# Performance work log

Measured on AMD Instinct MI355X. Metric: run time of the kernel, lower is better.

## Reference

```python
import jax, jax.numpy as jnp
import numpy as np

T_MAX, BATCH, NUM_CLASSES = 128, 64, 32
BEAM = 16
BLANK_DEC = NUM_CLASSES - 1   # TF ctc_beam_search_decoder uses num_classes-1 as blank
BLANK_PAD = 0                 # layer's blank_index: pad value for the dense output
NEG = -1e30                   # finite -inf substitute (avoids nan in logsumexp)


def setup_inputs():
    key = jax.random.key(0)
    k1, k2 = jax.random.split(key)
    data = jax.random.normal(k1, (T_MAX, BATCH, NUM_CLASSES), dtype=jnp.float32)
    data_length = jax.random.randint(k2, (BATCH,), T_MAX // 2, T_MAX + 1).astype(jnp.int32)
    return {"data": data, "data_length": data_length}


def _decode_one(logp_seq, length):
    """CTC prefix beam search (Graves) for one sample.
    logp_seq: [T, C] log-softmax scores. length: scalar int valid frames.
    Returns (dense prediction [T] padded with BLANK_PAD, log prob of best path).
    """
    Tt, Cc = logp_seq.shape
    L = Tt  # max decoded length
    bw = BEAM
    ar_b = jnp.arange(bw)
    ar_c = jnp.arange(Cc)
    ar_l = jnp.arange(L)

    prefixes0 = jnp.zeros((bw, L), jnp.int32)
    lens0 = jnp.zeros((bw,), jnp.int32)
    lp_b0 = jnp.full((bw,), NEG, jnp.float32).at[0].set(0.0)  # empty prefix, ends in blank
    lp_nb0 = jnp.full((bw,), NEG, jnp.float32)

    def step(state, inp):
        prefixes, lens, lp_b, lp_nb = state
        logp, t = inp
        lp_tot = jnp.logaddexp(lp_b, lp_nb)                      # [bw]
        valid = lp_tot > NEG / 2                                 # live beams (prefixes distinct)
        last = jnp.where(lens > 0, prefixes[ar_b, jnp.maximum(lens - 1, 0)], -1)

        # -- 'stay' candidates: prefix unchanged (emit blank, or repeat last char) --
        stay_lp_b = lp_tot + logp[BLANK_DEC]
        stay_lp_nb = jnp.where(lens > 0, lp_nb + logp[jnp.maximum(last, 0)], NEG)

        # -- 'extend' candidates ext[i, c]: prefix_i ++ [c], c != blank --
        # repeating last char only continues from the blank-ending mass
        ext = jnp.where(ar_c[None, :] == last[:, None], lp_b[:, None], lp_tot[:, None]) + logp[None, :]
        ext = ext.at[:, BLANK_DEC].set(NEG)

        # -- merge ext(i, c) into stay(j) when prefixes[j] == prefixes[i] ++ [c] --
        eq = prefixes[:, None, :] == prefixes[None, :, :]        # [i, j, L]
        maskp = ar_l[None, None, :] < lens[:, None, None]        # positions p < lens[i]
        pm = jnp.all(eq | ~maskp, axis=-1)                       # [i, j] prefix match up to lens[i]
        char_ji = prefixes[:, jnp.minimum(lens, L - 1)].T        # [i, j] = prefixes[j, lens[i]]
        match = (pm & (lens[None, :] == lens[:, None] + 1) & valid[None, :])[:, :, None] \
                & (char_ji[:, :, None] == ar_c[None, None, :])   # [i, j, C]
        merged = jax.nn.logsumexp(jnp.where(match, ext[:, None, :], NEG), axis=(0, 2))  # [j]
        stay_lp_nb = jnp.logaddexp(stay_lp_nb, merged)
        consumed = jnp.any(match, axis=1)                        # [i, C]
        ext = jnp.where(consumed, NEG, ext)

        # -- keep top beam_width candidates (all remaining prefixes are distinct) --
        stay_score = jnp.logaddexp(stay_lp_b, stay_lp_nb)        # [bw]
        scores = jnp.concatenate([stay_score, ext.reshape(-1)])  # [bw + bw*C]
        _, idx = jax.lax.top_k(scores, bw)
        is_ext = idx >= bw
        i_stay = jnp.minimum(idx, bw - 1)
        e = jnp.maximum(idx - bw, 0)
        i_ext, c_ext = e // Cc, e % Cc
        src = jnp.where(is_ext, i_ext, i_stay)
        base_pref = prefixes[src]                                # [bw, L]
        base_len = lens[src]
        new_pref = jnp.where(is_ext[:, None] & (ar_l[None, :] == base_len[:, None]),
                             c_ext[:, None].astype(jnp.int32), base_pref)
        new_len = base_len + is_ext.astype(jnp.int32)
        new_lp_b = jnp.where(is_ext, NEG, stay_lp_b[i_stay])
        new_lp_nb = jnp.where(is_ext, ext[i_ext, c_ext], stay_lp_nb[i_stay])

        # frames past this sample's length leave the state untouched
        active = t < length
        prefixes = jnp.where(active, new_pref, prefixes)
        lens = jnp.where(active, new_len, lens)
        lp_b = jnp.where(active, new_lp_b, lp_b)
        lp_nb = jnp.where(active, new_lp_nb, lp_nb)
        return (prefixes, lens, lp_b, lp_nb), None

    (prefixes, lens, lp_b, lp_nb), _ = jax.lax.scan(
        step, (prefixes0, lens0, lp_b0, lp_nb0), (logp_seq, jnp.arange(Tt)))

    # beam 0 is the most likely path (top_k keeps beams sorted by score);
    # dense output padded with blank_index, mirroring sparse.to_dense + pad
    pred = jnp.where(ar_l < lens[0], prefixes[0], BLANK_PAD)
    prob = jnp.logaddexp(lp_b[0], lp_nb[0])
    return pred, prob


def reference(data, data_length):
    # TF's ctc_beam_search_decoder applies softmax to the logits internally
    logp = jax.nn.log_softmax(data, axis=-1)                     # [T, B, C]
    preds, probs = jax.vmap(_decode_one, in_axes=(1, 0))(logp, data_length)
    # top_paths=1 -> _select_most_likely_path returns the single decoded path
    return preds                                                 # [B, T] int32
```

## Files before the change

kernel.cpp:

```cpp
#include <hip/hip_runtime.h>
#include <math.h>

#define T_MAXX 128
#define BATCHN 64
#define NC     32
#define NCP    33
#define BW     16
#define BLANKC 31
#define NEGF   (-1e30f)

typedef unsigned long long u64;
typedef unsigned int u32;

static const u64 PA_C = 0x100000001B3ULL;
static const u64 PB_C = 6364136223846793005ULL;

#define FENCE() asm volatile("" ::: "memory")

__device__ __forceinline__ float xexp(float x)  { return expf(x); }
__device__ __forceinline__ float xlog(float x)  { return logf(x); }
__device__ __forceinline__ float xlog1p(float x){ return log1pf(x); }

__device__ __forceinline__ float logaddexpf_(float a, float b) {
    float m = fmaxf(a, b);
    float d = fabsf(a - b);
    return m + xlog1p(xexp(-d));
}

template<int C>
__device__ __forceinline__ float fdpp_keep(float v) {
    return __int_as_float(__builtin_amdgcn_update_dpp(
        __float_as_int(v), __float_as_int(v), C, 0xF, 0xF, false));
}
template<int C>
__device__ __forceinline__ float fdpp_zero(float v) {
    return __int_as_float(__builtin_amdgcn_update_dpp(
        0, __float_as_int(v), C, 0xF, 0xF, true));
}
template<int C>
__device__ __forceinline__ u32 udpp_keep(u32 v) {
    return (u32)__builtin_amdgcn_update_dpp((int)v, (int)v, C, 0xF, 0xF, false);
}

__device__ __forceinline__ double dkey_pack(u32 u, u32 inv10) {
    u64 p = 0x3FF0000000000000ULL | ((u64)u << 10) | (u64)inv10;
    return __longlong_as_double((long long)p);
}
template<int C>
__device__ __forceinline__ double ddpp_keep(double v) {
    u64 b = (u64)__double_as_longlong(v);
    u32 lo = udpp_keep<C>((u32)b);
    u32 hi = udpp_keep<C>((u32)(b >> 32));
    return __longlong_as_double((long long)(((u64)hi << 32) | lo));
}
template<int P>
__device__ __forceinline__ double dswz(double v) {
    u64 b = (u64)__double_as_longlong(v);
    u32 lo = (u32)__builtin_amdgcn_ds_swizzle((int)(u32)b, P);
    u32 hi = (u32)__builtin_amdgcn_ds_swizzle((int)(u32)(b >> 32), P);
    return __longlong_as_double((long long)(((u64)hi << 32) | lo));
}
__device__ __forceinline__ double dbperm(double v, int srcl) {
    u64 b = (u64)__double_as_longlong(v);
    u32 lo = (u32)__builtin_amdgcn_ds_bpermute(srcl << 2, (int)(u32)b);
    u32 hi = (u32)__builtin_amdgcn_ds_bpermute(srcl << 2, (int)(u32)(b >> 32));
    return __longlong_as_double((long long)(((u64)hi << 32) | lo));
}
__device__ __forceinline__ double grp16_dmax(double m) {
    m = fmax(m, ddpp_keep<0xB1>(m));
    m = fmax(m, ddpp_keep<0x4E>(m));
    m = fmax(m, ddpp_keep<0x141>(m));
    m = fmax(m, ddpp_keep<0x140>(m));
    return m;
}
__device__ __forceinline__ void dce(double &m, double o, bool keepmax) {
    double mx = fmax(m, o), mn = fmin(m, o);
    m = keepmax ? mx : mn;
}

extern "C" __global__ void __launch_bounds__(64)
CTCPredictionsCpu_kernel(const float* __restrict__ data,
                         const int* __restrict__ dlen,
                         int* __restrict__ out)
{
    const int b      = blockIdx.x;
    const int tid    = threadIdx.x;
    const int length = dlen[b];
    const int lane_c = tid & 31;
    const int lane_h = tid >> 5;
    const int lane_g = tid & 15;
    const int grp    = tid >> 4;

    __shared__ float logpS[T_MAXX][NC];
    __shared__ float ext[BW][NCP];
    __shared__ int   lensS[BW], lastS[BW];
    __shared__ float lpBS[BW], lpTotS[BW];
    __shared__ u64   hAS[BW], hBS[BW];
    __shared__ u64   hAXS[BW], hBXS[BW];
    __shared__ int   trace[T_MAXX][BW];
    __shared__ int   outbuf[T_MAXX];

    #pragma unroll 4
    for (int f0 = 0; f0 < T_MAXX; f0 += 2) {
        int f = f0 + lane_h;
        float x = data[((size_t)f * BATCHN + b) * NC + lane_c];
        float mm = x;
        mm = fmaxf(mm, fdpp_keep<0xB1>(mm));
        mm = fmaxf(mm, fdpp_keep<0x4E>(mm));
        mm = fmaxf(mm, fdpp_keep<0x141>(mm));
        mm = fmaxf(mm, fdpp_keep<0x140>(mm));
        { float o = __int_as_float(
              __builtin_amdgcn_ds_swizzle(__float_as_int(mm), 0x401F));
          mm = fmaxf(mm, o); }
        float e = xexp(x - mm);
        float ss = e;
        ss += fdpp_zero<0xB1>(ss);
        ss += fdpp_zero<0x4E>(ss);
        ss += fdpp_zero<0x141>(ss);
        ss += fdpp_zero<0x140>(ss);
        { float o = __int_as_float(
              __builtin_amdgcn_ds_swizzle(__float_as_int(ss), 0x401F));
          ss += o; }
        float ls2 = xlog(ss);
        logpS[f][lane_c] = (x - mm) - ls2;
    }
    FENCE();

    int   myLen  = 0;
    int   myLast = -1;
    float myLpB  = (tid == 0) ? 0.0f : NEGF;
    float myLpNB = NEGF;
    u64   myHA   = 1, myHB = 1;

    for (int t = 0; t < length; ++t) {
        float mylogp  = logpS[t][lane_c];
        float lpBlank = logpS[t][BLANKC];

        float myTot = 0.0f, stayB = 0.0f, stayNB = 0.0f;
        if (tid < BW) {
            myTot = logaddexpf_(myLpB, myLpNB);
            float lp_last = logpS[t][(myLast >= 0) ? myLast : 0];
            stayB  = myTot + lpBlank;
            stayNB = (myLen > 0) ? (myLpNB + lp_last) : NEGF;
            lensS[tid]  = myLen;
            lastS[tid]  = myLast;
            lpBS[tid]   = myLpB;
            lpTotS[tid] = myTot;
            hAS[tid]    = myHA;
            hBS[tid]    = myHB;
            hAXS[tid]   = myHA * PA_C;
            hBXS[tid]   = myHB * PB_C;
        }
        FENCE();

        #pragma unroll
        for (int s8 = 0; s8 < 8; ++s8) {
            int i = 2 * s8 + lane_h;
            float base = (lane_c == lastS[i]) ? lpBS[i] : lpTotS[i];
            float v = base + mylogp;
            if (lane_c == BLANKC) v = NEGF;
            ext[i][lane_c] = v;
        }
        FENCE();

        float staySc = NEGF;
        if (tid < BW) {
            bool valid = myTot > -5e29f;
            if (valid && myLen > 0) {
                const int cj = myLast;
                const u64 wantA = myHA - (u64)(cj + 1);
                const u64 wantB = myHB - (u64)(cj + 1);
                u32 mmask = 0;
                #pragma unroll
                for (int i = 0; i < BW; ++i) {
                    bool hit = (hAXS[i] == wantA) && (hBXS[i] == wantB);
                    mmask |= hit ? (1u << i) : 0u;
                }
                if (mmask) {
                    int i0 = __ffs(mmask) - 1;
                    float merged = ext[i0][cj];
                    ext[i0][cj] = NEGF;
                    stayNB = logaddexpf_(stayNB, merged);
                }
            }
            staySc = logaddexpf_(stayB, stayNB);
        }
        FENCE();

        double K[9];
        #pragma unroll
        for (int j = 0; j < 8; ++j) {
            int r = 4 * grp + (j >> 1);
            int c = lane_g + ((j & 1) << 4);
            u32 uu = __float_as_uint(ext[r][c]);
            uu = (uu & 0x80000000u) ? ~uu : (uu | 0x80000000u);
            K[j] = dkey_pack(uu, 1023u - (u32)(BW + r * NC + c));
        }
        if (grp == 0) {
            u32 u = __float_as_uint(staySc);
            u = (u & 0x80000000u) ? ~u : (u | 0x80000000u);
            K[8] = dkey_pack(u, 1023u - (u32)lane_g);
        } else {
            K[8] = 0.0;
        }

        #define CE(a,bb) { double hi_ = fmax(K[a], K[bb]); \
                           double lo_ = fmin(K[a], K[bb]); \
                           K[a] = hi_; K[bb] = lo_; }
        CE(0,1) CE(2,3) CE(4,5) CE(6,7)
        CE(0,2) CE(1,3) CE(4,6) CE(5,7)
        CE(1,2) CE(5,6)
        CE(0,4) CE(1,5) CE(2,6) CE(3,7)
        CE(2,4) CE(3,5)
        CE(1,2) CE(3,4) CE(5,6)
        CE(7,8) CE(6,7) CE(5,6) CE(4,5) CE(3,4) CE(2,3) CE(1,2) CE(0,1)
        #undef CE

        double W = 0.0;
        #pragma unroll
        for (int k = 0; k < BW; ++k) {
            double best = grp16_dmax(K[0]);
            W = (lane_g == k) ? best : W;
            bool win = (K[0] == best);
            #pragma unroll
            for (int r = 0; r < 8; ++r) K[r] = win ? K[r + 1] : K[r];
            K[8] = win ? 0.0 : K[8];
        }

        { double o = dswz<0x7C1F>(W);    dce(W, o, (tid & 16) == 0); }
        { double o = dswz<0x201F>(W);    dce(W, o, (tid & 8)  == 0); }
        { double o = dswz<0x101F>(W);    dce(W, o, (tid & 4)  == 0); }
        { double o = ddpp_keep<0x4E>(W); dce(W, o, (tid & 2)  == 0); }
        { double o = ddpp_keep<0xB1>(W); dce(W, o, (tid & 1)  == 0); }
        {
            double o = dbperm(W, (tid + 16) & 63);
            W = (tid >= 16 && tid < 32) ? o : W;
        }
        { double o = dswz<0x7C1F>(W);    dce(W, o, (tid & 16) == 0); }
        { double o = dswz<0x201F>(W);    dce(W, o, (tid & 8)  == 0); }
        { double o = dswz<0x101F>(W);    dce(W, o, (tid & 4)  == 0); }
        { double o = ddpp_keep<0x4E>(W); dce(W, o, (tid & 2)  == 0); }
        { double o = ddpp_keep<0xB1>(W); dce(W, o, (tid & 1)  == 0); }
        int myidx = 1023 - (int)((u64)__double_as_longlong(W) & 1023ULL);

        bool isext = (tid < BW) && (myidx >= BW);
        int  istay = (tid < BW && !isext) ? myidx : 0;
        float gB  = __shfl(stayB,  istay, 32);
        float gNB = __shfl(stayNB, istay, 32);
        if (tid < BW) {
            int e2 = isext ? (myidx - BW) : 0;
            int ie = e2 >> 5, ce = e2 & 31;
            int src = isext ? ie : istay;
            int  sLen  = lensS[src];
            int  sLast = lastS[src];
            u64  sHA   = hAS[src], sHB = hBS[src];
            u64  sHAX  = hAXS[src], sHBX = hBXS[src];
            float extv = ext[ie][ce];
            myLen  = sLen + (isext ? 1 : 0);
            myLast = isext ? ce : sLast;
            myLpB  = isext ? NEGF : gB;
            myLpNB = isext ? extv : gNB;
            myHA   = isext ? (sHAX + (u64)(ce + 1)) : sHA;
            myHB   = isext ? (sHBX + (u64)(ce + 1)) : sHB;
            trace[t][tid] = src | (ce << 8) | (isext ? (1 << 16) : 0);
        }
        FENCE();
    }

    FENCE();
    for (int l = tid; l < T_MAXX; l += 64) outbuf[l] = 0;
    FENCE();
    if (tid == 0) {
        int cur = 0;
        int pos = myLen - 1;
        for (int s = length - 1; s >= 0; --s) {
            int e = trace[s][cur];
            if (e & (1 << 16)) outbuf[pos--] = (e >> 8) & 0xFF;
            cur = e & 0xFF;
        }
    }
    FENCE();
    for (int l = tid; l < T_MAXX; l += 64) out[b * T_MAXX + l] = outbuf[l];
}

extern "C" void kernel_launch(void* const* d_in, const int* in_sizes, int n_in,
                              void* d_out, int out_size, void* d_ws, size_t ws_size,
                              hipStream_t stream) {
    const float* data = (const float*)d_in[0];
    const int*   dlen = (const int*)d_in[1];
    int*         out  = (int*)d_out;
    hipLaunchKernelGGL(CTCPredictionsCpu_kernel, dim3(BATCHN), dim3(64), 0, stream,
                       data, dlen, out);
}
```

Baseline: 486.2 us.

## Replace iterative top-16 extraction with bitonic top-k merge across lanes

Replaces the 16-round serial extract-max loop and the subsequent cross-lane bitonic sort of winners with a per-lane sorted list of 16 keys, merged pairwise across lanes via DPP/swizzle/bpermute exchanges using a top-k bitonic merge and cleanup network. Each lane then picks its rank's key by binary selection. Stay scores are passed through shared memory instead of shuffles. This removes the 16 serialized reduction rounds but adds many more double compare-exchanges and cross-lane moves per merge stage, and increases register pressure.

Result: slower. 661.3 us (+36.0%).

```diff
diff --git a/kernel.cpp b/kernel.cpp
--- a/kernel.cpp
+++ b/kernel.cpp
@@ -65,17 +65,6 @@
     u32 lo = (u32)__builtin_amdgcn_ds_bpermute(srcl << 2, (int)(u32)b);
     u32 hi = (u32)__builtin_amdgcn_ds_bpermute(srcl << 2, (int)(u32)(b >> 32));
     return __longlong_as_double((long long)(((u64)hi << 32) | lo));
-}
-__device__ __forceinline__ double grp16_dmax(double m) {
-    m = fmax(m, ddpp_keep<0xB1>(m));
-    m = fmax(m, ddpp_keep<0x4E>(m));
-    m = fmax(m, ddpp_keep<0x141>(m));
-    m = fmax(m, ddpp_keep<0x140>(m));
-    return m;
-}
-__device__ __forceinline__ void dce(double &m, double o, bool keepmax) {
-    double mx = fmax(m, o), mn = fmin(m, o);
-    m = keepmax ? mx : mn;
 }
 
 extern "C" __global__ void __launch_bounds__(64)
@@ -95,6 +84,7 @@
     __shared__ float ext[BW][NCP];
     __shared__ int   lensS[BW], lastS[BW];
     __shared__ float lpBS[BW], lpTotS[BW];
+    __shared__ float stayBS[BW], stayNBS[BW];
     __shared__ u64   hAS[BW], hBS[BW];
     __shared__ u64   hAXS[BW], hBXS[BW];
     __shared__ int   trace[T_MAXX][BW];
@@ -146,6 +136,7 @@
             lastS[tid]  = myLast;
             lpBS[tid]   = myLpB;
             lpTotS[tid] = myTot;
+            stayBS[tid] = stayB;
             hAS[tid]    = myHA;
             hBS[tid]    = myHB;
             hAXS[tid]   = myHA * PA_C;
@@ -183,11 +174,12 @@
                     stayNB = logaddexpf_(stayNB, merged);
                 }
             }
+            stayNBS[tid] = stayNB;
             staySc = logaddexpf_(stayB, stayNB);
         }
         FENCE();
 
-        double K[9];
+        double K[16];
         #pragma unroll
         for (int j = 0; j < 8; ++j) {
             int r = 4 * grp + (j >> 1);
@@ -215,38 +207,61 @@
         CE(1,2) CE(3,4) CE(5,6)
         CE(7,8) CE(6,7) CE(5,6) CE(4,5) CE(3,4) CE(2,3) CE(1,2) CE(0,1)
         #undef CE
-
-        double W = 0.0;
-        #pragma unroll
-        for (int k = 0; k < BW; ++k) {
-            double best = grp16_dmax(K[0]);
-            W = (lane_g == k) ? best : W;
-            bool win = (K[0] == best);
+        #pragma unroll
+        for (int j = 9; j < 16; ++j) K[j] = 0.0;
+
+        #define CEM(a,bb) { double hi_ = fmax(M[a], M[bb]); \
+                            double lo_ = fmin(M[a], M[bb]); \
+                            M[a] = hi_; M[bb] = lo_; }
+        #define CLEANUP() \
+            CEM(0,8) CEM(1,9) CEM(2,10) CEM(3,11) CEM(4,12) CEM(5,13) CEM(6,14) CEM(7,15) \
+            CEM(0,4) CEM(1,5) CEM(2,6)  CEM(3,7)  CEM(8,12) CEM(9,13) CEM(10,14) CEM(11,15) \
+            CEM(0,2) CEM(1,3) CEM(4,6)  CEM(5,7)  CEM(8,10) CEM(9,11) CEM(12,14) CEM(13,15) \
+            CEM(0,1) CEM(2,3) CEM(4,5)  CEM(6,7)  CEM(8,9)  CEM(10,11) CEM(12,13) CEM(14,15)
+        #define MERGE_DPP(CTRL) { \
+            double M[16]; \
+            _Pragma("unroll") \
+            for (int i = 0; i < 16; ++i) M[i] = fmax(K[i], ddpp_keep<CTRL>(K[15 - i])); \
+            CLEANUP() \
+            _Pragma("unroll") \
+            for (int i = 0; i < 16; ++i) K[i] = M[i]; \
+        }
+        MERGE_DPP(0xB1)
+        MERGE_DPP(0x4E)
+        MERGE_DPP(0x141)
+        MERGE_DPP(0x140)
+        {
+            double M[16];
             #pragma unroll
-            for (int r = 0; r < 8; ++r) K[r] = win ? K[r + 1] : K[r];
-            K[8] = win ? 0.0 : K[8];
-        }
-
-        { double o = dswz<0x7C1F>(W);    dce(W, o, (tid & 16) == 0); }
-        { double o = dswz<0x201F>(W);    dce(W, o, (tid & 8)  == 0); }
-        { double o = dswz<0x101F>(W);    dce(W, o, (tid & 4)  == 0); }
-        { double o = ddpp_keep<0x4E>(W); dce(W, o, (tid & 2)  == 0); }
-        { double o = ddpp_keep<0xB1>(W); dce(W, o, (tid & 1)  == 0); }
+            for (int i = 0; i < 16; ++i) M[i] = fmax(K[i], dswz<0x401F>(K[15 - i]));
+            CLEANUP()
+            #pragma unroll
+            for (int i = 0; i < 16; ++i) K[i] = M[i];
+        }
         {
-            double o = dbperm(W, (tid + 16) & 63);
-            W = (tid >= 16 && tid < 32) ? o : W;
-        }
-        { double o = dswz<0x7C1F>(W);    dce(W, o, (tid & 16) == 0); }
-        { double o = dswz<0x201F>(W);    dce(W, o, (tid & 8)  == 0); }
-        { double o = dswz<0x101F>(W);    dce(W, o, (tid & 4)  == 0); }
-        { double o = ddpp_keep<0x4E>(W); dce(W, o, (tid & 2)  == 0); }
-        { double o = ddpp_keep<0xB1>(W); dce(W, o, (tid & 1)  == 0); }
-        int myidx = 1023 - (int)((u64)__double_as_longlong(W) & 1023ULL);
+            double M[16];
+            #pragma unroll
+            for (int i = 0; i < 16; ++i) M[i] = fmax(K[i], dbperm(K[15 - i], tid ^ 32));
+            CLEANUP()
+            #pragma unroll
+            for (int i = 0; i < 16; ++i) K[i] = M[i];
+        }
+        #undef MERGE_DPP
+        #undef CLEANUP
+        #undef CEM
+
+        double T8[8], T4[4], T2[2], Tw;
+        #pragma unroll
+        for (int i = 0; i < 8; ++i) T8[i] = (lane_g & 8) ? K[i + 8] : K[i];
+        #pragma unroll
+        for (int i = 0; i < 4; ++i) T4[i] = (lane_g & 4) ? T8[i + 4] : T8[i];
+        #pragma unroll
+        for (int i = 0; i < 2; ++i) T2[i] = (lane_g & 2) ? T4[i + 2] : T4[i];
+        Tw = (lane_g & 1) ? T2[1] : T2[0];
+        int myidx = 1023 - (int)((u64)__double_as_longlong(Tw) & 1023ULL);
 
         bool isext = (tid < BW) && (myidx >= BW);
         int  istay = (tid < BW && !isext) ? myidx : 0;
-        float gB  = __shfl(stayB,  istay, 32);
-        float gNB = __shfl(stayNB, istay, 32);
         if (tid < BW) {
             int e2 = isext ? (myidx - BW) : 0;
             int ie = e2 >> 5, ce = e2 & 31;
@@ -256,6 +271,8 @@
             u64  sHA   = hAS[src], sHB = hBS[src];
             u64  sHAX  = hAXS[src], sHBX = hBXS[src];
             float extv = ext[ie][ce];
+            float gB   = stayBS[istay];
+            float gNB  = stayNBS[istay];
             myLen  = sLen + (isext ? 1 : 0);
             myLast = isext ? ce : sLast;
             myLpB  = isext ? NEGF : gB;
```

## Pack per-beam state into vector LDS structs, drop second hash, prefetch next logp row

Applied to the files above, without the earlier changes.

Per-beam scalars (last, lpB, lpTot, len) are packed into an int4 and the hash pair into a ulonglong2, so each beam's state is read with one wide LDS load. The second prefix hash and the validity check in merge detection are dropped, leaving a single 64-bit hash compare. Blank logp now comes from a readlane instead of LDS, and the next timestep's logp row is prefetched into a register. The ext rows are read as float2 with padding of 34, and the top-k selection loop skips shifts on already-exhausted key slots. The cost is a higher chance of hash collisions from using one hash, and a different LDS access pattern.

Measured after the change: 450.7 us. -7.3%, faster.

```diff
diff --git a/kernel.cpp b/kernel.cpp
--- a/kernel.cpp
+++ b/kernel.cpp
@@ -4,7 +4,7 @@
 #define T_MAXX 128
 #define BATCHN 64
 #define NC     32
-#define NCP    33
+#define NCP    34
 #define BW     16
 #define BLANKC 31
 #define NEGF   (-1e30f)
@@ -13,7 +13,6 @@
 typedef unsigned int u32;
 
 static const u64 PA_C = 0x100000001B3ULL;
-static const u64 PB_C = 6364136223846793005ULL;
 
 #define FENCE() asm volatile("" ::: "memory")
 
@@ -45,6 +44,10 @@
 __device__ __forceinline__ double dkey_pack(u32 u, u32 inv10) {
     u64 p = 0x3FF0000000000000ULL | ((u64)u << 10) | (u64)inv10;
     return __longlong_as_double((long long)p);
+}
+__device__ __forceinline__ u32 score_bits(float sc) {
+    u32 u = __float_as_uint(sc);
+    return (u & 0x80000000u) ? ~u : (u | 0x80000000u);
 }
 template<int C>
 __device__ __forceinline__ double ddpp_keep(double v) {
@@ -93,10 +96,9 @@
 
     __shared__ float logpS[T_MAXX][NC];
     __shared__ float ext[BW][NCP];
-    __shared__ int   lensS[BW], lastS[BW];
-    __shared__ float lpBS[BW], lpTotS[BW];
-    __shared__ u64   hAS[BW], hBS[BW];
-    __shared__ u64   hAXS[BW], hBXS[BW];
+    __shared__ int4  S4[BW];
+    __shared__ ulonglong2 HH[BW];
+    __shared__ float stayBS[BW], stayNBS[BW];
     __shared__ int   trace[T_MAXX][BW];
     __shared__ int   outbuf[T_MAXX];
 
@@ -130,11 +132,16 @@
     int   myLast = -1;
     float myLpB  = (tid == 0) ? 0.0f : NEGF;
     float myLpNB = NEGF;
-    u64   myHA   = 1, myHB = 1;
+    u64   myHA   = 1;
+
+    float lp_cur = logpS[0][lane_c];
 
     for (int t = 0; t < length; ++t) {
-        float mylogp  = logpS[t][lane_c];
-        float lpBlank = logpS[t][BLANKC];
+        float mylogp  = lp_cur;
+        float lpBlank = __int_as_float(
+            __builtin_amdgcn_readlane(__float_as_int(mylogp), 31));
+        int   tn      = (t + 1 < length) ? t + 1 : t;
+        float lp_nxt  = logpS[tn][lane_c];
 
         float myTot = 0.0f, stayB = 0.0f, stayNB = 0.0f;
         if (tid < BW) {
@@ -142,21 +149,19 @@
             float lp_last = logpS[t][(myLast >= 0) ? myLast : 0];
             stayB  = myTot + lpBlank;
             stayNB = (myLen > 0) ? (myLpNB + lp_last) : NEGF;
-            lensS[tid]  = myLen;
-            lastS[tid]  = myLast;
-            lpBS[tid]   = myLpB;
-            lpTotS[tid] = myTot;
-            hAS[tid]    = myHA;
-            hBS[tid]    = myHB;
-            hAXS[tid]   = myHA * PA_C;
-            hBXS[tid]   = myHB * PB_C;
+            S4[tid] = make_int4(myLast, __float_as_int(myLpB),
+                                __float_as_int(myTot), myLen);
+            HH[tid] = make_ulonglong2(myHA, myHA * PA_C);
+            stayBS[tid] = stayB;
         }
         FENCE();
 
         #pragma unroll
         for (int s8 = 0; s8 < 8; ++s8) {
             int i = 2 * s8 + lane_h;
-            float base = (lane_c == lastS[i]) ? lpBS[i] : lpTotS[i];
+            int4 s = S4[i];
+            float base = (lane_c == s.x) ? __int_as_float(s.y)
+                                         : __int_as_float(s.z);
             float v = base + mylogp;
             if (lane_c == BLANKC) v = NEGF;
             ext[i][lane_c] = v;
@@ -165,15 +170,13 @@
 
         float staySc = NEGF;
         if (tid < BW) {
-            bool valid = myTot > -5e29f;
-            if (valid && myLen > 0) {
+            if (myLen > 0) {
                 const int cj = myLast;
-                const u64 wantA = myHA - (u64)(cj + 1);
-                const u64 wantB = myHB - (u64)(cj + 1);
+                const u64 want = myHA - (u64)(cj + 1);
                 u32 mmask = 0;
                 #pragma unroll
                 for (int i = 0; i < BW; ++i) {
-                    bool hit = (hAXS[i] == wantA) && (hBXS[i] == wantB);
+                    bool hit = (HH[i].y == want);
                     mmask |= hit ? (1u << i) : 0u;
                 }
                 if (mmask) {
@@ -183,26 +186,24 @@
                     stayNB = logaddexpf_(stayNB, merged);
                 }
             }
+            stayNBS[tid] = stayNB;
             staySc = logaddexpf_(stayB, stayNB);
         }
         FENCE();
 
         double K[9];
         #pragma unroll
-        for (int j = 0; j < 8; ++j) {
-            int r = 4 * grp + (j >> 1);
-            int c = lane_g + ((j & 1) << 4);
-            u32 uu = __float_as_uint(ext[r][c]);
-            uu = (uu & 0x80000000u) ? ~uu : (uu | 0x80000000u);
-            K[j] = dkey_pack(uu, 1023u - (u32)(BW + r * NC + c));
-        }
-        if (grp == 0) {
-            u32 u = __float_as_uint(staySc);
-            u = (u & 0x80000000u) ? ~u : (u | 0x80000000u);
-            K[8] = dkey_pack(u, 1023u - (u32)lane_g);
-        } else {
-            K[8] = 0.0;
-        }
+        for (int rr = 0; rr < 4; ++rr) {
+            int r = 4 * grp + rr;
+            float2 p = *(const float2*)&ext[r][2 * lane_g];
+            int c0 = 2 * lane_g;
+            K[2 * rr]     = dkey_pack(score_bits(p.x),
+                                      1023u - (u32)(BW + r * NC + c0));
+            K[2 * rr + 1] = dkey_pack(score_bits(p.y),
+                                      1023u - (u32)(BW + r * NC + c0 + 1));
+        }
+        K[8] = (grp == 0) ? dkey_pack(score_bits(staySc), 1023u - (u32)lane_g)
+                          : 0.0;
 
         #define CE(a,bb) { double hi_ = fmax(K[a], K[bb]); \
                            double lo_ = fmin(K[a], K[bb]); \
@@ -222,9 +223,11 @@
             double best = grp16_dmax(K[0]);
             W = (lane_g == k) ? best : W;
             bool win = (K[0] == best);
+            const int d = (k < 8) ? 8 : (15 - k);
             #pragma unroll
-            for (int r = 0; r < 8; ++r) K[r] = win ? K[r + 1] : K[r];
-            K[8] = win ? 0.0 : K[8];
+            for (int r = 0; r < 8; ++r)
+                if (r < d) K[r] = win ? K[r + 1] : K[r];
+            if (k < 15) K[d] = win ? 0.0 : K[d];
         }
 
         { double o = dswz<0x7C1F>(W);    dce(W, o, (tid & 16) == 0); }
@@ -245,26 +248,25 @@
 
         bool isext = (tid < BW) && (myidx >= BW);
         int  istay = (tid < BW && !isext) ? myidx : 0;
-        float gB  = __shfl(stayB,  istay, 32);
-        float gNB = __shfl(stayNB, istay, 32);
         if (tid < BW) {
             int e2 = isext ? (myidx - BW) : 0;
             int ie = e2 >> 5, ce = e2 & 31;
             int src = isext ? ie : istay;
-            int  sLen  = lensS[src];
-            int  sLast = lastS[src];
-            u64  sHA   = hAS[src], sHB = hBS[src];
-            u64  sHAX  = hAXS[src], sHBX = hBXS[src];
+            int4       s  = S4[src];
+            ulonglong2 hh = HH[src];
             float extv = ext[ie][ce];
-            myLen  = sLen + (isext ? 1 : 0);
-            myLast = isext ? ce : sLast;
+            float gB   = stayBS[istay];
+            float gNB  = stayNBS[istay];
+            myLen  = s.w + (isext ? 1 : 0);
+            myLast = isext ? ce : s.x;
             myLpB  = isext ? NEGF : gB;
             myLpNB = isext ? extv : gNB;
-            myHA   = isext ? (sHAX + (u64)(ce + 1)) : sHA;
-            myHB   = isext ? (sHBX + (u64)(ce + 1)) : sHB;
+            myHA   = isext ? (hh.y + (u64)(ce + 1)) : hh.x;
             trace[t][tid] = src | (ce << 8) | (isext ? (1 << 16) : 0);
         }
         FENCE();
+
+        lp_cur = lp_nxt;
     }
 
     FENCE();
```
